# Optimization experiments

Measured on AMD Instinct MI355X. Metric: run time of the kernel, lower is better.

The kernel has to match this reference:

```python
import jax, jax.numpy as jnp
import numpy as np
from jax import lax

T = 16384          # num_tokens
H = 512            # hidden_size
HC = 4             # hc_mult
NGRAM = 4          # max_ngram_size -> conv dilation
N_EMBED = 256      # n_embed_per_ngram
N_HEADPN = 4       # n_head_per_ngram
NUM_HEADS = (NGRAM - 1) * N_HEADPN          # 12 embedding heads
HEAD_DIM = N_EMBED // N_HEADPN              # 64
E = (NGRAM - 1) * N_EMBED                   # 768 = engram_hidden_size
VOCAB = 50000
K = 4              # conv kernel_size
EPS = 1e-5         # layernorm_eps
GATE_EPS = 1e-6


def setup_inputs() -> dict:
    key = jax.random.key(0)
    ks = jax.random.split(key, 8)
    hash_ids = jax.random.randint(ks[0], (T, NUM_HEADS), 0, VOCAB, dtype=jnp.int32)
    offsets = jnp.asarray(np.concatenate([[0], np.cumsum([VOCAB] * (NUM_HEADS - 1))]).astype(np.int32))
    embedding_weight = jax.random.normal(ks[1], (NUM_HEADS * VOCAB, HEAD_DIM), jnp.float32) * 0.02
    key_projs_w = jax.random.normal(ks[2], (HC, E, H), jnp.float32) * 0.02
    q_norm_w = jnp.ones((HC, H), jnp.float32)
    k_norm_w = jnp.ones((HC, H), jnp.float32)
    v_proj_w = jax.random.normal(ks[3], (E, H), jnp.float32) * 0.02
    conv_w = jax.random.normal(ks[4], (HC * H, K), jnp.float32) * 0.1
    conv_norm_w = jnp.ones((HC, H), jnp.float32)
    hidden_states = jax.random.normal(ks[5], (T, HC, H), jnp.float32)
    return {
        'hash_ids': hash_ids, 'offsets': offsets, 'embedding_weight': embedding_weight,
        'key_projs_w': key_projs_w, 'q_norm_w': q_norm_w, 'k_norm_w': k_norm_w,
        'v_proj_w': v_proj_w, 'conv_w': conv_w, 'conv_norm_w': conv_norm_w,
        'hidden_states': hidden_states,
    }


def _group_rms_norm(x, w, eps=EPS):
    # x: [G, T, H], w: [G, H]; RMS over last dim, per-group affine scale
    inv = lax.rsqrt(jnp.mean(x * x, axis=-1, keepdims=True) + eps)
    return x * inv * w[:, None, :]


def reference(hash_ids, offsets, embedding_weight, key_projs_w, q_norm_w, k_norm_w,
              v_proj_w, conv_w, conv_norm_w, hidden_states):
    num_tokens, hc_mult, hidden = hidden_states.shape
    # --- MultiHeadEmbedding: hash-indexed gather into a concatenated table ---
    emb = embedding_weight[hash_ids + offsets[None, :]]          # [T, NUM_HEADS, HEAD_DIM]
    emb = emb.reshape(num_tokens, E)                              # [T, E]
    # --- key projection per hc group (bmm) ---
    keys = jnp.einsum('te,geh->gth', emb, key_projs_w)            # [HC, T, H]
    key_n = _group_rms_norm(keys, k_norm_w)
    query_n = _group_rms_norm(hidden_states.transpose(1, 0, 2), q_norm_w)  # [HC, T, H]
    # --- scaled dot-product gate ---
    scale = 1.0 / jnp.sqrt(jnp.asarray(hidden, hidden_states.dtype))
    gate = jax.nn.sigmoid(jnp.sum(key_n * query_n, axis=-1) * scale)       # [HC, T]
    gate = gate.T[:, :, None]                                     # [T, HC, 1]
    # --- value projection + gating ---
    value = gate * (emb @ v_proj_w)[:, None, :]                   # [T, HC, H]
    # --- ShortConv: GroupRMSNorm + depthwise dilated causal conv1d + SiLU ---
    x_n = _group_rms_norm(value.transpose(1, 0, 2), conv_norm_w)  # [HC, T, H]
    x_bct = x_n.transpose(0, 2, 1).reshape(1, hc_mult * hidden, num_tokens)  # [1, C, T]
    pad = NGRAM * (K - 1)
    y = lax.conv_general_dilated(
        x_bct, conv_w[:, None, :],                                # kernel [C, 1, K]
        window_strides=(1,), padding=[(pad, 0)], rhs_dilation=(NGRAM,),
        feature_group_count=hc_mult * hidden,
        dimension_numbers=('NCH', 'OIH', 'NCH'))
    y = jax.nn.silu(y)[0]                                         # [C, T]
    y = y.reshape(hc_mult, hidden, num_tokens).transpose(2, 0, 1) # [T, HC, H]
    return value + y


if __name__ == '__main__':
    out = reference(**setup_inputs())
    print(out.shape, out.dtype)
```

## Files before the change

### kernel.cpp

```cpp
#include <hip/hip_runtime.h>
#include <hip/hip_bf16.h>
#include <math.h>

#define T_TOK  16384
#define H_DIM  512
#define NHEADS 12
#define E_DIM  768
#define EPS_N  1e-5f
#define QK_SCALE 0.04419417382415922f

typedef unsigned short u16;
typedef __bf16 bf16;
typedef bf16   bf16x8 __attribute__((ext_vector_type(8)));
typedef float  f32x4  __attribute__((ext_vector_type(4)));
typedef u16    u16x4  __attribute__((ext_vector_type(4)));
typedef u16    u16x8  __attribute__((ext_vector_type(8)));

__device__ __forceinline__ u16 f2bf(float f) {
  unsigned u = __builtin_bit_cast(unsigned, f);
  unsigned r = u + 0x7fffu + ((u >> 16) & 1u);
  return (u16)(r >> 16);
}
__device__ __forceinline__ float bf2f(u16 h) {
  unsigned u = ((unsigned)h) << 16;
  return __builtin_bit_cast(float, u);
}

__global__ __launch_bounds__(256) void prep_all(
    const int* __restrict__ hash_ids, const int* __restrict__ offsets,
    const float* __restrict__ emb_w, u16* __restrict__ emb,
    const float* __restrict__ kp, const float* __restrict__ vp,
    u16* __restrict__ wt,
    const float* __restrict__ conv_w, const float* __restrict__ cnw,
    const float* __restrict__ qw, const float* __restrict__ kw,
    float* __restrict__ wc, float* __restrict__ qwkw) {
  __shared__ float tile[32][33];
  int b = blockIdx.x, tid = threadIdx.x;
  if (b < 6144) {
    int idx = b * 256 + tid;
    int pair = idx >> 3;
    int sub = idx & 7;
    int t = pair / 12;
    int head = pair - t * 12;
    int row = hash_ids[pair] + offsets[head];
    const float* src = emb_w + (size_t)row * 64 + sub * 8;
    float4 a = *(const float4*)src;
    float4 c = *(const float4*)(src + 4);
    u16x8 o;
    o[0] = f2bf(a.x); o[1] = f2bf(a.y); o[2] = f2bf(a.z); o[3] = f2bf(a.w);
    o[4] = f2bf(c.x); o[5] = f2bf(c.y); o[6] = f2bf(c.z); o[7] = f2bf(c.w);
    *(u16x8*)(emb + (size_t)t * E_DIM + head * 64 + sub * 8) = o;
  } else if (b < 8064) {
    int i = b - 6144;
    int m = i / 384;
    int rem = i - m * 384;
    int h0 = (rem & 15) * 32, e0 = (rem >> 4) * 32;
    const float* src = (m < 4) ? (kp + (size_t)m * E_DIM * H_DIM) : vp;
    int tx = tid & 31, ty = tid >> 5;
    #pragma unroll
    for (int j = 0; j < 32; j += 8)
      tile[ty + j][tx] = src[(size_t)(e0 + ty + j) * H_DIM + h0 + tx];
    __syncthreads();
    #pragma unroll
    for (int j = 0; j < 32; j += 8) {
      int h = h0 + ty + j, e = e0 + tx;
      wt[(size_t)(m * H_DIM + h) * E_DIM + e] = f2bf(tile[tx][ty + j]);
    }
  } else {
    #pragma unroll
    for (int c8 = 0; c8 < 8; ++c8) {
      int cf = c8 * 256 + tid;
      float c = cnw[cf];
      #pragma unroll
      for (int k = 0; k < 4; ++k) wc[k * 2048 + cf] = conv_w[cf * 4 + k] * c;
      qwkw[cf] = qw[cf] * kw[cf];
    }
  }
}

__global__ __launch_bounds__(256, 2) void gemm_bf16(
    const u16* __restrict__ A, const u16* __restrict__ BT,
    const float* __restrict__ hidden, const float* __restrict__ qwkw,
    u16* __restrict__ V, float* __restrict__ kssP, float* __restrict__ qkP,
    float* __restrict__ qssP, float* __restrict__ msvP) {
  __shared__ __align__(16) char smem[33792];
  u16 (*As)[64] = (u16(*)[64])smem;
  u16 (*Bs)[64] = (u16(*)[64])(smem + 16384);
  u16*    qlds  = (u16*)smem;
  float2* red2h = (float2*)smem;
  float*  red1  = (float*)smem;
  const int K = E_DIM;
  int tid = threadIdx.x;
  int lane = tid & 63, wid = tid >> 6;

  int orig = blockIdx.x + blockIdx.y * 20;
  int swz = (orig & 7) * 320 + (orig >> 3);
  int bx = swz % 20, by = swz / 20;

  int wm = (wid >> 1) * 64, wn = (wid & 1) * 64;
  int widN = wid & 1;
  int lr16 = lane & 15, rgrp = lane >> 4;
  int swz8 = lr16 & 7;

  int srow = tid >> 3;
  int sunit = ((tid & 7) ^ (srow & 7)) * 8;
  const u16* aptr = A + (size_t)(by * 128 + srow) * K + sunit;
  const u16* bptr = BT + (size_t)(bx * 128 + srow) * K + sunit;
  int lds_off = tid * 16;

  f32x4 acc[4][4] = {};

  for (int k0 = 0; k0 < K; k0 += 64) {
    #pragma unroll
    for (int r = 0; r < 4; ++r) {
      __builtin_amdgcn_global_load_lds(
        (const __attribute__((address_space(1))) void*)(aptr + (size_t)(r * 32) * K + k0),
        (__attribute__((address_space(3))) void*)(smem + r * 4096 + lds_off),
        16, 0, 0);
      __builtin_amdgcn_global_load_lds(
        (const __attribute__((address_space(1))) void*)(bptr + (size_t)(r * 32) * K + k0),
        (__attribute__((address_space(3))) void*)(smem + 16384 + r * 4096 + lds_off),
        16, 0, 0);
    }
    __syncthreads();
    #pragma unroll
    for (int kk = 0; kk < 2; ++kk) {
      int un = ((kk * 4 + rgrp) ^ swz8) * 8;
      bf16x8 af[4], bfv[4];
      #pragma unroll
      for (int m = 0; m < 4; ++m)
        af[m] = *reinterpret_cast<const bf16x8*>(&As[wm + m * 16 + lr16][un]);
      #pragma unroll
      for (int n = 0; n < 4; ++n)
        bfv[n] = *reinterpret_cast<const bf16x8*>(&Bs[wn + n * 16 + lr16][un]);
      #pragma unroll
      for (int m = 0; m < 4; ++m)
        #pragma unroll
        for (int n = 0; n < 4; ++n)
          acc[m][n] = __builtin_amdgcn_mfma_f32_16x16x32_bf16(af[m], bfv[n], acc[m][n], 0, 0, 0);
    }
    __syncthreads();
  }

  if (bx < 16) {
    int g = bx >> 2, qq = bx & 3;
    const float* hq = hidden + (size_t)(by * 128) * 2048 + g * 512 + qq * 128;
    float s2[8];
    #pragma unroll
    for (int p = 0; p < 8; ++p) {
      int row = p * 16 + (tid >> 4);
      int col = (tid & 15) * 8;
      const float* src = hq + (size_t)row * 2048 + col;
      float4 x0 = *(const float4*)src;
      float4 x1 = *(const float4*)(src + 4);
      float qv[8] = {x0.x, x0.y, x0.z, x0.w, x1.x, x1.y, x1.z, x1.w};
      u16x8 o;
      float ss = 0.f;
      #pragma unroll
      for (int j = 0; j < 8; ++j) { ss += qv[j] * qv[j]; o[j] = f2bf(qv[j]); }
      s2[p] = ss;
      *(u16x8*)&qlds[row * 132 + col] = o;
    }
    #pragma unroll
    for (int off = 1; off < 16; off <<= 1)
      #pragma unroll
      for (int p = 0; p < 8; ++p) s2[p] += __shfl_xor(s2[p], off, 64);
    if ((tid & 15) == 0) {
      #pragma unroll
      for (int p = 0; p < 8; ++p) {
        int t = by * 128 + p * 16 + (tid >> 4);
        qssP[(t * 4 + g) * 4 + qq] = s2[p];
      }
    }
    __syncthreads();

    int colg = g * 512 + qq * 128 + wn + lr16;
    float w4[4];
    #pragma unroll
    for (int n = 0; n < 4; ++n) w4[n] = qwkw[colg + n * 16];
    float sk2r[16], sqkr[16];
    #pragma unroll
    for (int m = 0; m < 4; ++m) {
      #pragma unroll
      for (int j = 0; j < 4; ++j) {
        int r = wm + m * 16 + rgrp * 4 + j;
        float sk2 = 0.f, sqk = 0.f;
        #pragma unroll
        for (int n = 0; n < 4; ++n) {
          float kv = acc[m][n][j];
          float qv = bf2f(qlds[r * 132 + wn + n * 16 + lr16]);
          sk2 += kv * kv;
          sqk += qv * w4[n] * kv;
        }
        sk2 += __shfl_xor(sk2, 8, 64);
        sqk += __shfl_xor(sqk, 8, 64);
        sk2r[m * 4 + j] = sk2;
        sqkr[m * 4 + j] = sqk;
      }
    }
    __syncthreads();
    if (lr16 < 8) {
      #pragma unroll
      for (int m = 0; m < 4; ++m)
        #pragma unroll
        for (int j = 0; j < 4; ++j) {
          int r = wm + m * 16 + rgrp * 4 + j;
          red2h[(widN * 128 + r) * 8 + lr16] =
              make_float2(sk2r[m * 4 + j], sqkr[m * 4 + j]);
        }
    }
    __syncthreads();
    if (tid < 128) {
      float s0 = 0.f, s1 = 0.f;
      #pragma unroll
      for (int j = 0; j < 8; ++j) {
        int jj = (j + tid) & 7;
        float2 a = red2h[tid * 8 + jj];
        float2 b = red2h[(128 + tid) * 8 + jj];
        s0 += a.x + b.x;
        s1 += a.y + b.y;
      }
      int t = by * 128 + tid;
      int o = (t * 4 + g) * 4 + qq;
      kssP[o] = s0;
      qkP[o]  = s1;
    }
  } else {
    int q2i = bx - 16;
    #pragma unroll
    for (int m = 0; m < 4; ++m) {
      #pragma unroll
      for (int j = 0; j < 4; ++j) {
        int r = wm + m * 16 + rgrp * 4 + j;
        size_t t = (size_t)(by * 128 + r);
        float sv2 = 0.f;
        #pragma unroll
        for (int n = 0; n < 4; ++n) {
          float v = acc[m][n][j];
          sv2 += v * v;
          V[t * 512 + q2i * 128 + wn + n * 16 + lr16] = f2bf(v);
        }
        red1[(widN * 128 + r) * 16 + lr16] = sv2;
      }
    }
    __syncthreads();
    if (tid < 128) {
      float s = 0.f;
      #pragma unroll
      for (int j = 0; j < 16; ++j) {
        int jj = (j + tid) & 15;
        s += red1[tid * 16 + jj] + red1[(128 + tid) * 16 + jj];
      }
      int t = by * 128 + tid;
      msvP[t * 4 + q2i] = s;
    }
  }
}

__global__ __launch_bounds__(256) void gate_finish(
    const float* __restrict__ kssP, const float* __restrict__ qkP,
    const float* __restrict__ qssP, const float* __restrict__ msvP,
    float* __restrict__ gateA, float* __restrict__ aA) {
  int i = blockIdx.x * 256 + threadIdx.x;
  int t = i >> 2;
  float4 k4 = *(const float4*)&kssP[i * 4];
  float4 d4 = *(const float4*)&qkP[i * 4];
  float4 q4 = *(const float4*)&qssP[i * 4];
  float4 m4 = *(const float4*)&msvP[t * 4];
  float kss = k4.x + k4.y + k4.z + k4.w;
  float qk  = d4.x + d4.y + d4.z + d4.w;
  float qss = q4.x + q4.y + q4.z + q4.w;
  float msv = (m4.x + m4.y + m4.z + m4.w) * (1.0f / 512.0f);
  float qinv = rsqrtf(qss * (1.0f / 512.0f) + EPS_N);
  float kinv = rsqrtf(kss * (1.0f / 512.0f) + EPS_N);
  float gate = 1.0f / (1.0f + __expf(-qk * qinv * kinv * QK_SCALE));
  gateA[i] = gate;
  aA[i] = gate * rsqrtf(gate * gate * msv + EPS_N);
}

__global__ __launch_bounds__(256) void out_kernel(
    const u16* __restrict__ V,
    const float* __restrict__ gateA, const float* __restrict__ aA,
    const float* __restrict__ wc,
    float* __restrict__ out) {
  int idx = blockIdx.x * 256 + threadIdx.x;
  int t = idx >> 8;
  int c8 = (idx & 255) * 8;
  int g = c8 >> 9;
  int h = c8 & 511;

  float acc[8] = {0.f, 0.f, 0.f, 0.f, 0.f, 0.f, 0.f, 0.f};
  float vr_t[8];
  #pragma unroll
  for (int k = 0; k < 4; ++k) {
    int tk = t - 12 + 4 * k;
    if (tk < 0) continue;
    float s = aA[tk * 4 + g];
    u16x8 vv = *(const u16x8*)&V[(size_t)tk * 512 + h];
    float4 w0 = *(const float4*)(wc + k * 2048 + c8);
    float4 w1 = *(const float4*)(wc + k * 2048 + c8 + 4);
    float w8[8] = {w0.x, w0.y, w0.z, w0.w, w1.x, w1.y, w1.z, w1.w};
    #pragma unroll
    for (int j = 0; j < 8; ++j) {
      float v = bf2f(vv[j]);
      acc[j] += w8[j] * s * v;
      if (k == 3) vr_t[j] = v;
    }
  }
  float gate = gateA[t * 4 + g];
  float r[8];
  #pragma unroll
  for (int j = 0; j < 8; ++j) {
    float y = acc[j];
    r[j] = gate * vr_t[j] + y / (1.0f + __expf(-y));
  }
  float* op = out + (size_t)t * 2048 + c8;
  *(float4*)op       = make_float4(r[0], r[1], r[2], r[3]);
  *(float4*)(op + 4) = make_float4(r[4], r[5], r[6], r[7]);
}

extern "C" void kernel_launch(void* const* d_in, const int* in_sizes, int n_in,
                              void* d_out, int out_size, void* d_ws, size_t ws_size,
                              hipStream_t stream) {
  const int*   hash_ids = (const int*)d_in[0];
  const int*   offsets  = (const int*)d_in[1];
  const float* emb_w    = (const float*)d_in[2];
  const float* kp       = (const float*)d_in[3];
  const float* qw       = (const float*)d_in[4];
  const float* kw       = (const float*)d_in[5];
  const float* vp       = (const float*)d_in[6];
  const float* conv_w   = (const float*)d_in[7];
  const float* cw       = (const float*)d_in[8];
  const float* hidden   = (const float*)d_in[9];
  float* out = (float*)d_out;
  char*  ws  = (char*)d_ws;

  u16*   V     = (u16*)ws;
  u16*   emb   = (u16*)(ws + 16777216);
  u16*   wt    = (u16*)(ws + 41943040);
  float* kssP  = (float*)(ws + 45875200);
  float* qkP   = (float*)(ws + 46923776);
  float* qssP  = (float*)(ws + 47972352);
  float* msvP  = (float*)(ws + 49020928);
  float* gateA = (float*)(ws + 49283072);
  float* aA    = (float*)(ws + 49545216);
  float* wc    = (float*)(ws + 49807360);
  float* qwkw  = (float*)(ws + 49840128);

  prep_all<<<8065, 256, 0, stream>>>(hash_ids, offsets, emb_w, emb,
                                     kp, vp, wt, conv_w, cw, qw, kw, wc, qwkw);
  gemm_bf16<<<dim3(20, 128), 256, 0, stream>>>(emb, wt, hidden, qwkw,
                                               V, kssP, qkP, qssP, msvP);
  gate_finish<<<(T_TOK * 4) / 256, 256, 0, stream>>>(kssP, qkP, qssP, msvP, gateA, aA);
  out_kernel<<<T_TOK * 256 / 256, 256, 0, stream>>>(V, gateA, aA, wc, out);
}
```

Baseline: 165.5 us.

## Replace in-block LDS reduction with per-wave partial writes reduced in gate_finish

The GEMM epilogue for the key blocks no longer runs a two-barrier shared-memory reduction of per-row key sum-of-squares and q·k. Each wave now shuffle-reduces its values further and writes float2 partials straight to global memory, and gate_finish sums the 32 partials per token/group. The q staging buffer switches from padded rows to an XOR swizzle, which shrinks LDS to 32 KB. In exchange, global partial traffic grows by roughly 16 MB of writes plus the matching reads in gate_finish.

```diff
diff --git a/kernel.cpp b/kernel.cpp
--- a/kernel.cpp
+++ b/kernel.cpp
@@ -81,13 +81,12 @@
 __global__ __launch_bounds__(256, 2) void gemm_bf16(
     const u16* __restrict__ A, const u16* __restrict__ BT,
     const float* __restrict__ hidden, const float* __restrict__ qwkw,
-    u16* __restrict__ V, float* __restrict__ kssP, float* __restrict__ qkP,
+    u16* __restrict__ V, float2* __restrict__ kqP,
     float* __restrict__ qssP, float* __restrict__ msvP) {
-  __shared__ __align__(16) char smem[33792];
+  __shared__ __align__(16) char smem[32768];
   u16 (*As)[64] = (u16(*)[64])smem;
   u16 (*Bs)[64] = (u16(*)[64])(smem + 16384);
   u16*    qlds  = (u16*)smem;
-  float2* red2h = (float2*)smem;
   float*  red1  = (float*)smem;
   const int K = E_DIM;
   int tid = threadIdx.x;
@@ -145,12 +144,13 @@
   if (bx < 16) {
     int g = bx >> 2, qq = bx & 3;
     const float* hq = hidden + (size_t)(by * 128) * 2048 + g * 512 + qq * 128;
+    int rxw = (((tid >> 4) >> 2) & 3) << 4;
     float s2[8];
     #pragma unroll
     for (int p = 0; p < 8; ++p) {
       int row = p * 16 + (tid >> 4);
-      int col = (tid & 15) * 8;
-      const float* src = hq + (size_t)row * 2048 + col;
+      int c0 = (tid & 15) * 8;
+      const float* src = hq + (size_t)row * 2048 + c0;
       float4 x0 = *(const float4*)src;
       float4 x1 = *(const float4*)(src + 4);
       float qv[8] = {x0.x, x0.y, x0.z, x0.w, x1.x, x1.y, x1.z, x1.w};
@@ -159,7 +159,7 @@
       #pragma unroll
       for (int j = 0; j < 8; ++j) { ss += qv[j] * qv[j]; o[j] = f2bf(qv[j]); }
       s2[p] = ss;
-      *(u16x8*)&qlds[row * 132 + col] = o;
+      *(u16x8*)&qlds[row * 128 + (c0 ^ rxw)] = o;
     }
     #pragma unroll
     for (int off = 1; off < 16; off <<= 1)
@@ -178,7 +178,7 @@
     float w4[4];
     #pragma unroll
     for (int n = 0; n < 4; ++n) w4[n] = qwkw[colg + n * 16];
-    float sk2r[16], sqkr[16];
+    int rxr = rgrp << 4;
     #pragma unroll
     for (int m = 0; m < 4; ++m) {
       #pragma unroll
@@ -188,42 +188,20 @@
         #pragma unroll
         for (int n = 0; n < 4; ++n) {
           float kv = acc[m][n][j];
-          float qv = bf2f(qlds[r * 132 + wn + n * 16 + lr16]);
+          float qv = bf2f(qlds[r * 128 + ((wn + n * 16 + lr16) ^ rxr)]);
           sk2 += kv * kv;
           sqk += qv * w4[n] * kv;
         }
         sk2 += __shfl_xor(sk2, 8, 64);
         sqk += __shfl_xor(sqk, 8, 64);
-        sk2r[m * 4 + j] = sk2;
-        sqkr[m * 4 + j] = sqk;
+        sk2 += __shfl_xor(sk2, 4, 64);
+        sqk += __shfl_xor(sqk, 4, 64);
+        if (lr16 < 4) {
+          int t = by * 128 + r;
+          kqP[((size_t)(t * 4 + g) * 4 + qq) * 8 + widN * 4 + lr16] =
+              make_float2(sk2, sqk);
+        }
       }
-    }
-    __syncthreads();
-    if (lr16 < 8) {
-      #pragma unroll
-      for (int m = 0; m < 4; ++m)
-        #pragma unroll
-        for (int j = 0; j < 4; ++j) {
-          int r = wm + m * 16 + rgrp * 4 + j;
-          red2h[(widN * 128 + r) * 8 + lr16] =
-              make_float2(sk2r[m * 4 + j], sqkr[m * 4 + j]);
-        }
-    }
-    __syncthreads();
-    if (tid < 128) {
-      float s0 = 0.f, s1 = 0.f;
-      #pragma unroll
-      for (int j = 0; j < 8; ++j) {
-        int jj = (j + tid) & 7;
-        float2 a = red2h[tid * 8 + jj];
-        float2 b = red2h[(128 + tid) * 8 + jj];
-        s0 += a.x + b.x;
-        s1 += a.y + b.y;
-      }
-      int t = by * 128 + tid;
-      int o = (t * 4 + g) * 4 + qq;
-      kssP[o] = s0;
-      qkP[o]  = s1;
     }
   } else {
     int q2i = bx - 16;
@@ -258,17 +236,21 @@
 }
 
 __global__ __launch_bounds__(256) void gate_finish(
-    const float* __restrict__ kssP, const float* __restrict__ qkP,
-    const float* __restrict__ qssP, const float* __restrict__ msvP,
+    const float2* __restrict__ kqP, const float* __restrict__ qssP,
+    const float* __restrict__ msvP,
     float* __restrict__ gateA, float* __restrict__ aA) {
   int i = blockIdx.x * 256 + threadIdx.x;
   int t = i >> 2;
-  float4 k4 = *(const float4*)&kssP[i * 4];
-  float4 d4 = *(const float4*)&qkP[i * 4];
+  const float4* pf = (const float4*)(kqP + (size_t)i * 32);
+  float kss = 0.f, qk = 0.f;
+  #pragma unroll
+  for (int u = 0; u < 16; ++u) {
+    float4 f = pf[u];
+    kss += f.x + f.z;
+    qk  += f.y + f.w;
+  }
   float4 q4 = *(const float4*)&qssP[i * 4];
   float4 m4 = *(const float4*)&msvP[t * 4];
-  float kss = k4.x + k4.y + k4.z + k4.w;
-  float qk  = d4.x + d4.y + d4.z + d4.w;
   float qss = q4.x + q4.y + q4.z + q4.w;
   float msv = (m4.x + m4.y + m4.z + m4.w) * (1.0f / 512.0f);
   float qinv = rsqrtf(qss * (1.0f / 512.0f) + EPS_N);
@@ -335,22 +317,21 @@
   float* out = (float*)d_out;
   char*  ws  = (char*)d_ws;
 
-  u16*   V     = (u16*)ws;
-  u16*   emb   = (u16*)(ws + 16777216);
-  u16*   wt    = (u16*)(ws + 41943040);
-  float* kssP  = (float*)(ws + 45875200);
-  float* qkP   = (float*)(ws + 46923776);
-  float* qssP  = (float*)(ws + 47972352);
-  float* msvP  = (float*)(ws + 49020928);
-  float* gateA = (float*)(ws + 49283072);
-  float* aA    = (float*)(ws + 49545216);
-  float* wc    = (float*)(ws + 49807360);
-  float* qwkw  = (float*)(ws + 49840128);
+  u16*    V     = (u16*)ws;
+  u16*    emb   = (u16*)(ws + 16777216);
+  u16*    wt    = (u16*)(ws + 41943040);
+  float2* kqP   = (float2*)(ws + 45875200);
+  float*  qssP  = (float*)(ws + 62652416);
+  float*  msvP  = (float*)(ws + 63700992);
+  float*  gateA = (float*)(ws + 63963136);
+  float*  aA    = (float*)(ws + 64225280);
+  float*  wc    = (float*)(ws + 64487424);
+  float*  qwkw  = (float*)(ws + 64520192);
 
   prep_all<<<8065, 256, 0, stream>>>(hash_ids, offsets, emb_w, emb,
                                      kp, vp, wt, conv_w, cw, qw, kw, wc, qwkw);
   gemm_bf16<<<dim3(20, 128), 256, 0, stream>>>(emb, wt, hidden, qwkw,
-                                               V, kssP, qkP, qssP, msvP);
-  gate_finish<<<(T_TOK * 4) / 256, 256, 0, stream>>>(kssP, qkP, qssP, msvP, gateA, aA);
+                                               V, kqP, qssP, msvP);
+  gate_finish<<<(T_TOK * 4) / 256, 256, 0, stream>>>(kqP, qssP, msvP, gateA, aA);
   out_kernel<<<T_TOK * 256 / 256, 256, 0, stream>>>(V, gateA, aA, wc, out);
 }
```

New measurement: 172.2 us. +4.1%, slower.

## Restructure GEMM into 256x128 tiles with triple-buffered async LDS pipeline

Applied to the files above, without the earlier changes.

The GEMM block grows from 128x128 tiles with 256 threads to 256x128 tiles with 512 threads. It uses a three-stage ring of LDS buffers filled by global_load_lds, with explicit vmcnt waits and barriers so loads for step k+2 overlap MFMA work on step k. MFMA phases run at raised priority via setprio. The hidden-state loads for the q-norm epilogue are interleaved into the main loop and held in registers, hiding their latency. The cost is 144KB of LDS per block and hand-tuned waitcnt counts that must exactly match the number of issued loads, which risks low occupancy and fragile correctness.

```diff
diff --git a/kernel.cpp b/kernel.cpp
--- a/kernel.cpp
+++ b/kernel.cpp
@@ -78,88 +78,137 @@
   }
 }
 
-__global__ __launch_bounds__(256, 2) void gemm_bf16(
+__global__ __launch_bounds__(512, 2) void gemm_bf16(
     const u16* __restrict__ A, const u16* __restrict__ BT,
     const float* __restrict__ hidden, const float* __restrict__ qwkw,
     u16* __restrict__ V, float* __restrict__ kssP, float* __restrict__ qkP,
     float* __restrict__ qssP, float* __restrict__ msvP) {
-  __shared__ __align__(16) char smem[33792];
-  u16 (*As)[64] = (u16(*)[64])smem;
-  u16 (*Bs)[64] = (u16(*)[64])(smem + 16384);
-  u16*    qlds  = (u16*)smem;
-  float2* red2h = (float2*)smem;
-  float*  red1  = (float*)smem;
+  __shared__ __align__(16) char smem[147456];
   const int K = E_DIM;
   int tid = threadIdx.x;
-  int lane = tid & 63, wid = tid >> 6;
-
-  int orig = blockIdx.x + blockIdx.y * 20;
-  int swz = (orig & 7) * 320 + (orig >> 3);
-  int bx = swz % 20, by = swz / 20;
-
-  int wm = (wid >> 1) * 64, wn = (wid & 1) * 64;
-  int widN = wid & 1;
+  int lane = tid & 63;
+  int wid = tid >> 6;
+  int wr = wid >> 1, wcl = wid & 1;
   int lr16 = lane & 15, rgrp = lane >> 4;
   int swz8 = lr16 & 7;
 
-  int srow = tid >> 3;
-  int sunit = ((tid & 7) ^ (srow & 7)) * 8;
-  const u16* aptr = A + (size_t)(by * 128 + srow) * K + sunit;
-  const u16* bptr = BT + (size_t)(bx * 128 + srow) * K + sunit;
-  int lds_off = tid * 16;
+  int orig = blockIdx.x + blockIdx.y * 20;
+  int swz = (orig & 7) * 160 + (orig >> 3);
+  int bx = swz % 20, by = swz / 20;
+  bool isKey = bx < 16;
+  int g = bx >> 2, qq = bx & 3;
+
+  int sunit = ((tid & 7) ^ ((tid >> 3) & 7)) * 8;
+  const u16* Abase = A + (size_t)(by * 256 + (tid >> 3)) * K + sunit;
+  const u16* Bbase = BT + (size_t)(bx * 128 + (tid >> 3)) * K + sunit;
+  int dstA = tid * 16;
+
+#define STGA(kt2, bs, r) __builtin_amdgcn_global_load_lds( \
+    (const __attribute__((address_space(1))) void*)(Abase + (size_t)((r) * 64) * K + (kt2) * 64), \
+    (__attribute__((address_space(3))) void*)(smem + (bs) * 49152 + (r) * 8192 + dstA), 16, 0, 0)
+#define STGB(kt2, bs, r) __builtin_amdgcn_global_load_lds( \
+    (const __attribute__((address_space(1))) void*)(Bbase + (size_t)((r) * 64) * K + (kt2) * 64), \
+    (__attribute__((address_space(3))) void*)(smem + (bs) * 49152 + 32768 + (r) * 8192 + dstA), 16, 0, 0)
+#define BAR    asm volatile("s_barrier" ::: "memory")
+#define CFENCE asm volatile("" ::: "memory")
+#define VMW(n) asm volatile("s_waitcnt vmcnt(" #n ")" ::: "memory")
 
   f32x4 acc[4][4] = {};
-
-  for (int k0 = 0; k0 < K; k0 += 64) {
-    #pragma unroll
-    for (int r = 0; r < 4; ++r) {
-      __builtin_amdgcn_global_load_lds(
-        (const __attribute__((address_space(1))) void*)(aptr + (size_t)(r * 32) * K + k0),
-        (__attribute__((address_space(3))) void*)(smem + r * 4096 + lds_off),
-        16, 0, 0);
-      __builtin_amdgcn_global_load_lds(
-        (const __attribute__((address_space(1))) void*)(bptr + (size_t)(r * 32) * K + k0),
-        (__attribute__((address_space(3))) void*)(smem + 16384 + r * 4096 + lds_off),
-        16, 0, 0);
-    }
-    __syncthreads();
+  float4 hA[8], hB[8];
+
+  STGA(0, 0, 0); STGA(0, 0, 1); STGA(0, 0, 2); STGA(0, 0, 3);
+  STGB(0, 0, 0); STGB(0, 0, 1);
+  STGA(1, 1, 0); STGA(1, 1, 1); STGA(1, 1, 2); STGA(1, 1, 3);
+  STGB(1, 1, 0); STGB(1, 1, 1);
+  VMW(6);
+  BAR;
+
+  int arow = (wr * 64 + lr16) * 64;
+  int brow = (wcl * 64 + lr16) * 64;
+
+  #pragma unroll
+  for (int kt = 0; kt < 12; ++kt) {
+    int br = kt % 3, bs = (kt + 2) % 3;
+    const u16* Ab = (const u16*)(smem + br * 49152);
+    const u16* Bb = (const u16*)(smem + br * 49152 + 32768);
+    bf16x8 fA[2][2], fB[4][2], fA2[2][2];
     #pragma unroll
     for (int kk = 0; kk < 2; ++kk) {
       int un = ((kk * 4 + rgrp) ^ swz8) * 8;
-      bf16x8 af[4], bfv[4];
-      #pragma unroll
-      for (int m = 0; m < 4; ++m)
-        af[m] = *reinterpret_cast<const bf16x8*>(&As[wm + m * 16 + lr16][un]);
+      fA[0][kk] = *(const bf16x8*)&Ab[arow + 0 * 1024 + un];
+      fA[1][kk] = *(const bf16x8*)&Ab[arow + 1 * 1024 + un];
+      fB[0][kk] = *(const bf16x8*)&Bb[brow + 0 * 1024 + un];
+      fB[1][kk] = *(const bf16x8*)&Bb[brow + 1 * 1024 + un];
+      fB[2][kk] = *(const bf16x8*)&Bb[brow + 2 * 1024 + un];
+      fB[3][kk] = *(const bf16x8*)&Bb[brow + 3 * 1024 + un];
+    }
+    if (kt < 10) { STGA(kt + 2, bs, 0); STGA(kt + 2, bs, 1); STGA(kt + 2, bs, 2); }
+    BAR;
+    __builtin_amdgcn_s_setprio(1);
+    #pragma unroll
+    for (int m = 0; m < 2; ++m)
       #pragma unroll
       for (int n = 0; n < 4; ++n)
-        bfv[n] = *reinterpret_cast<const bf16x8*>(&Bs[wn + n * 16 + lr16][un]);
-      #pragma unroll
-      for (int m = 0; m < 4; ++m)
         #pragma unroll
-        for (int n = 0; n < 4; ++n)
-          acc[m][n] = __builtin_amdgcn_mfma_f32_16x16x32_bf16(af[m], bfv[n], acc[m][n], 0, 0, 0);
-    }
-    __syncthreads();
-  }
-
-  if (bx < 16) {
-    int g = bx >> 2, qq = bx & 3;
-    const float* hq = hidden + (size_t)(by * 128) * 2048 + g * 512 + qq * 128;
+        for (int kk = 0; kk < 2; ++kk)
+          acc[m][n] = __builtin_amdgcn_mfma_f32_16x16x32_bf16(fA[m][kk], fB[n][kk], acc[m][n], 0, 0, 0);
+    __builtin_amdgcn_s_setprio(0);
+    BAR;
+    #pragma unroll
+    for (int kk = 0; kk < 2; ++kk) {
+      int un = ((kk * 4 + rgrp) ^ swz8) * 8;
+      fA2[0][kk] = *(const bf16x8*)&Ab[arow + 2 * 1024 + un];
+      fA2[1][kk] = *(const bf16x8*)&Ab[arow + 3 * 1024 + un];
+    }
+    if (kt < 10) { STGA(kt + 2, bs, 3); STGB(kt + 2, bs, 0); STGB(kt + 2, bs, 1); }
+    CFENCE;
+    if (isKey && kt < 8) {
+      int hrow = kt * 32 + (tid >> 4);
+      const float* hsrc = hidden + (size_t)(by * 256 + hrow) * 2048 +
+                          g * 512 + qq * 128 + (tid & 15) * 8;
+      hA[kt] = *(const float4*)hsrc;
+      hB[kt] = *(const float4*)(hsrc + 4);
+    }
+    CFENCE;
+    BAR;
+    __builtin_amdgcn_s_setprio(1);
+    #pragma unroll
+    for (int m = 0; m < 2; ++m)
+      #pragma unroll
+      for (int n = 0; n < 4; ++n)
+        #pragma unroll
+        for (int kk = 0; kk < 2; ++kk)
+          acc[m + 2][n] = __builtin_amdgcn_mfma_f32_16x16x32_bf16(fA2[m][kk], fB[n][kk], acc[m + 2][n], 0, 0, 0);
+    __builtin_amdgcn_s_setprio(0);
+    if (isKey) {
+      if (kt == 0) { VMW(8); }
+      else if (kt <= 7) { VMW(10); }
+      else if (kt == 8) { VMW(8); }
+      else if (kt == 9) { VMW(6); }
+      else if (kt == 10) { VMW(0); }
+    } else {
+      if (kt <= 9) { VMW(6); }
+      else if (kt == 10) { VMW(0); }
+    }
+    BAR;
+  }
+
+  __syncthreads();
+  if (isKey) {
+    u16*    qlds = (u16*)smem;
+    float2* red2 = (float2*)(smem + 98304);
     float s2[8];
     #pragma unroll
     for (int p = 0; p < 8; ++p) {
-      int row = p * 16 + (tid >> 4);
-      int col = (tid & 15) * 8;
-      const float* src = hq + (size_t)row * 2048 + col;
-      float4 x0 = *(const float4*)src;
-      float4 x1 = *(const float4*)(src + 4);
+      float4 x0 = hA[p], x1 = hB[p];
       float qv[8] = {x0.x, x0.y, x0.z, x0.w, x1.x, x1.y, x1.z, x1.w};
       u16x8 o;
       float ss = 0.f;
       #pragma unroll
       for (int j = 0; j < 8; ++j) { ss += qv[j] * qv[j]; o[j] = f2bf(qv[j]); }
       s2[p] = ss;
-      *(u16x8*)&qlds[row * 132 + col] = o;
+      int row = p * 32 + (tid >> 4);
+      *(u16x8*)&qlds[row * 132 + (tid & 15) * 8] = o;
     }
     #pragma unroll
     for (int off = 1; off < 16; off <<= 1)
@@ -168,93 +217,84 @@
     if ((tid & 15) == 0) {
       #pragma unroll
       for (int p = 0; p < 8; ++p) {
-        int t = by * 128 + p * 16 + (tid >> 4);
+        int t = by * 256 + p * 32 + (tid >> 4);
         qssP[(t * 4 + g) * 4 + qq] = s2[p];
       }
     }
     __syncthreads();
 
-    int colg = g * 512 + qq * 128 + wn + lr16;
     float w4[4];
     #pragma unroll
-    for (int n = 0; n < 4; ++n) w4[n] = qwkw[colg + n * 16];
-    float sk2r[16], sqkr[16];
+    for (int n = 0; n < 4; ++n)
+      w4[n] = qwkw[g * 512 + qq * 128 + wcl * 64 + n * 16 + lr16];
     #pragma unroll
     for (int m = 0; m < 4; ++m) {
       #pragma unroll
       for (int j = 0; j < 4; ++j) {
-        int r = wm + m * 16 + rgrp * 4 + j;
+        int r = wr * 64 + m * 16 + rgrp * 4 + j;
         float sk2 = 0.f, sqk = 0.f;
         #pragma unroll
         for (int n = 0; n < 4; ++n) {
           float kv = acc[m][n][j];
-          float qv = bf2f(qlds[r * 132 + wn + n * 16 + lr16]);
+          float qv = bf2f(qlds[r * 132 + wcl * 64 + n * 16 + lr16]);
           sk2 += kv * kv;
           sqk += qv * w4[n] * kv;
         }
         sk2 += __shfl_xor(sk2, 8, 64);
         sqk += __shfl_xor(sqk, 8, 64);
-        sk2r[m * 4 + j] = sk2;
-        sqkr[m * 4 + j] = sqk;
+        if (lr16 < 8) red2[(wcl * 256 + r) * 8 + lr16] = make_float2(sk2, sqk);
       }
     }
     __syncthreads();
-    if (lr16 < 8) {
-      #pragma unroll
-      for (int m = 0; m < 4; ++m)
-        #pragma unroll
-        for (int j = 0; j < 4; ++j) {
-          int r = wm + m * 16 + rgrp * 4 + j;
-          red2h[(widN * 128 + r) * 8 + lr16] =
-              make_float2(sk2r[m * 4 + j], sqkr[m * 4 + j]);
-        }
-    }
-    __syncthreads();
-    if (tid < 128) {
+    if (tid < 256) {
       float s0 = 0.f, s1 = 0.f;
       #pragma unroll
       for (int j = 0; j < 8; ++j) {
         int jj = (j + tid) & 7;
-        float2 a = red2h[tid * 8 + jj];
-        float2 b = red2h[(128 + tid) * 8 + jj];
+        float2 a = red2[tid * 8 + jj];
+        float2 b = red2[(256 + tid) * 8 + jj];
         s0 += a.x + b.x;
         s1 += a.y + b.y;
       }
-      int t = by * 128 + tid;
-      int o = (t * 4 + g) * 4 + qq;
+      int o = ((by * 256 + tid) * 4 + g) * 4 + qq;
       kssP[o] = s0;
       qkP[o]  = s1;
     }
   } else {
+    float* red1 = (float*)smem;
     int q2i = bx - 16;
     #pragma unroll
     for (int m = 0; m < 4; ++m) {
       #pragma unroll
       for (int j = 0; j < 4; ++j) {
-        int r = wm + m * 16 + rgrp * 4 + j;
-        size_t t = (size_t)(by * 128 + r);
+        int r = wr * 64 + m * 16 + rgrp * 4 + j;
+        size_t t = (size_t)(by * 256 + r);
         float sv2 = 0.f;
         #pragma unroll
         for (int n = 0; n < 4; ++n) {
           float v = acc[m][n][j];
           sv2 += v * v;
-          V[t * 512 + q2i * 128 + wn + n * 16 + lr16] = f2bf(v);
+          V[t * 512 + q2i * 128 + wcl * 64 + n * 16 + lr16] = f2bf(v);
         }
-        red1[(widN * 128 + r) * 16 + lr16] = sv2;
+        red1[(wcl * 256 + r) * 16 + lr16] = sv2;
       }
     }
     __syncthreads();
-    if (tid < 128) {
+    if (tid < 256) {
       float s = 0.f;
       #pragma unroll
       for (int j = 0; j < 16; ++j) {
         int jj = (j + tid) & 15;
-        s += red1[tid * 16 + jj] + red1[(128 + tid) * 16 + jj];
-      }
-      int t = by * 128 + tid;
-      msvP[t * 4 + q2i] = s;
-    }
-  }
+        s += red1[tid * 16 + jj] + red1[(256 + tid) * 16 + jj];
+      }
+      msvP[(by * 256 + tid) * 4 + q2i] = s;
+    }
+  }
+#undef STGA
+#undef STGB
+#undef BAR
+#undef CFENCE
+#undef VMW
 }
 
 __global__ __launch_bounds__(256) void gate_finish(
@@ -349,8 +389,8 @@
 
   prep_all<<<8065, 256, 0, stream>>>(hash_ids, offsets, emb_w, emb,
                                      kp, vp, wt, conv_w, cw, qw, kw, wc, qwkw);
-  gemm_bf16<<<dim3(20, 128), 256, 0, stream>>>(emb, wt, hidden, qwkw,
-                                               V, kssP, qkP, qssP, msvP);
+  gemm_bf16<<<dim3(20, 64), 512, 0, stream>>>(emb, wt, hidden, qwkw,
+                                              V, kssP, qkP, qssP, msvP);
   gate_finish<<<(T_TOK * 4) / 256, 256, 0, stream>>>(kssP, qkP, qssP, msvP, gateA, aA);
   out_kernel<<<T_TOK * 256 / 256, 256, 0, stream>>>(V, gateA, aA, wc, out);
 }
```

Result: no change. 165.5 us (+0.1%).
